# Performance work log

Measured on AMD Instinct MI355X. Metric: run time of the kernel, lower is better.

Reference implementation:

```python
import jax, jax.numpy as jnp
import numpy as np

N_NODES = 50000


def setup_inputs() -> dict:
    key = jax.random.key(0)
    k1, k2, k3, k4, k5 = jax.random.split(key, 5)
    x = jax.random.normal(k1, (N_NODES, 128), dtype=jnp.float32)
    edge_index = jax.random.randint(k2, (2, 800000), 0, N_NODES, dtype=jnp.int64)
    # Linear layers: torch Linear stores weight as [out, in]; init ~ U(-1/sqrt(in), 1/sqrt(in))
    s = 1.0 / np.sqrt(128.0)
    W_rel = jax.random.uniform(k3, (128, 128), dtype=jnp.float32, minval=-s, maxval=s)
    b_rel = jax.random.uniform(k4, (128,), dtype=jnp.float32, minval=-s, maxval=s)
    W_root = jax.random.uniform(k5, (128, 128), dtype=jnp.float32, minval=-s, maxval=s)
    return {"x": x, "edge_index": edge_index, "W_rel": W_rel, "b_rel": b_rel, "W_root": W_root}


def reference(x, edge_index, W_rel, b_rel, W_root):
    # GraphConv (PyG): out_i = W_rel @ (sum_{j -> i} x_j) + b_rel + W_root @ x_i
    src, dst = edge_index[0], edge_index[1]
    msgs = x[src]  # [E, in] gather
    agg = jax.ops.segment_sum(msgs, dst, num_segments=N_NODES)  # [N, in] scatter-add
    out = agg @ W_rel.T + b_rel + x @ W_root.T
    # ReLU; dropout_rate = DropoutRate.NONE -> p=0, identity
    return jax.nn.relu(out)
```

## Files before the change

### kernel.cpp

```cpp
#include <hip/hip_runtime.h>
#include <hip/hip_bf16.h>


#define F 128
#define NPB 32
#define NPARTS 8
#define CAP 128
#define CAPB 768
#define AST 68

typedef __bf16 bf16x8 __attribute__((ext_vector_type(8)));
typedef float f32x4 __attribute__((ext_vector_type(4)));

__device__ inline unsigned f32_to_bf16_rne(float f) {
  unsigned u = __float_as_uint(f);
  unsigned r = u + 0x7fffu + ((u >> 16) & 1u);
  return r >> 16;
}
__device__ inline unsigned pack2(float2 v) {
  return f32_to_bf16_rne(v.x) | (f32_to_bf16_rne(v.y) << 16);
}
__device__ inline unsigned pack2f(float a, float b) {
  return f32_to_bf16_rne(a) | (f32_to_bf16_rne(b) << 16);
}
__device__ inline void upk4(uint4 v, float* a) {
  a[0] += __uint_as_float(v.x << 16);
  a[1] += __uint_as_float(v.x & 0xffff0000u);
  a[2] += __uint_as_float(v.y << 16);
  a[3] += __uint_as_float(v.y & 0xffff0000u);
  a[4] += __uint_as_float(v.z << 16);
  a[5] += __uint_as_float(v.z & 0xffff0000u);
  a[6] += __uint_as_float(v.w << 16);
  a[7] += __uint_as_float(v.w & 0xffff0000u);
}

__global__ __launch_bounds__(256) void prep_bin2_kernel(
    const float4* __restrict__ x, const float2* __restrict__ w0,
    const float2* __restrict__ w1, const int* __restrict__ ei,
    uint2* __restrict__ xb2, unsigned* __restrict__ wb,
    int* __restrict__ binCursor, unsigned* __restrict__ bin,
    int E, int NB, int n4x, int n2w) {
  const int tid0 = blockIdx.x * 256 + threadIdx.x;
  const int stride = gridDim.x * 256;

  const int part = blockIdx.x & (NPARTS - 1);
  for (int e = tid0; e < E; e += stride) {
    unsigned src = (unsigned)ei[e];
    unsigned dst = (unsigned)ei[E + e];
    int cell = part * NB + (int)(dst >> 5);
    int slot = atomicAdd(&binCursor[cell], 1);
    if (slot < CAP) bin[(size_t)cell * CAP + slot] = (dst << 16) | src;
  }
  for (int i = tid0; i < n4x; i += stride) {
    float4 v = x[i];
    xb2[i] = make_uint2(pack2f(v.x, v.y), pack2f(v.z, v.w));
  }
  for (int i = tid0; i < 2 * n2w; i += stride)
    wb[i] = (i < n2w) ? pack2(w0[i]) : pack2(w1[i - n2w]);
}

__global__ __launch_bounds__(256) void agg_gemm2_kernel(
    const unsigned* __restrict__ xb, const unsigned* __restrict__ bin,
    const int* __restrict__ binCursor, const __bf16* __restrict__ wb,
    const float* __restrict__ brel, float* __restrict__ out, int N, int NB) {
  __shared__ int cntS[NPB];
  __shared__ int offS[NPB];
  __shared__ int curS[NPB];
  __shared__ unsigned short eLds[CAPB];
  __shared__ unsigned aLds[NPB * AST];

  const int b = blockIdx.x;
  const int t = threadIdx.x;
  if (t < NPB) cntS[t] = 0;
  __syncthreads();

  unsigned kreg[NPARTS];
  int cnt_p[NPARTS];
#pragma unroll
  for (int p = 0; p < NPARTS; ++p) {
    int cell = p * NB + b;
    int c = min(binCursor[cell], CAP);
    cnt_p[p] = c;
    kreg[p] = (t < c) ? bin[(size_t)cell * CAP + t] : 0u;
  }
#pragma unroll
  for (int p = 0; p < NPARTS; ++p) {
    if (t < cnt_p[p]) atomicAdd(&cntS[(kreg[p] >> 16) & (NPB - 1)], 1);
  }
  __syncthreads();

  if (t < 64) {
    int v = (t < NPB) ? cntS[t] : 0;
    int incl = v;
#pragma unroll
    for (int off = 1; off < NPB; off <<= 1) {
      int u = __shfl_up(incl, off);
      if (t >= off) incl += u;
    }
    if (t < NPB) {
      offS[t] = incl - v;
      curS[t] = incl - v;
    }
  }
  __syncthreads();

#pragma unroll
  for (int p = 0; p < NPARTS; ++p) {
    if (t < cnt_p[p]) {
      int d = (kreg[p] >> 16) & (NPB - 1);
      int pos = atomicAdd(&curS[d], 1);
      if (pos < CAPB) eLds[pos] = (unsigned short)(kreg[p] & 0xffffu);
    }
  }
  __syncthreads();

  const int wave = t >> 6;
  const int lane = t & 63;
  const int grp = lane >> 4;
  const int l16 = lane & 15;
  const uint4* __restrict__ xb4 = (const uint4*)xb;
  const int nodeBase = b * NPB;
  for (int di = wave; di < NPB; di += 4) {
    float a8[8] = {0.f, 0.f, 0.f, 0.f, 0.f, 0.f, 0.f, 0.f};
    int beg = min(offS[di], CAPB);
    int end = min(offS[di] + cntS[di], CAPB);
    int e = beg;
    for (; e + 16 <= end; e += 16) {
      int s0 = eLds[e + grp];
      int s1 = eLds[e + 4 + grp];
      int s2 = eLds[e + 8 + grp];
      int s3 = eLds[e + 12 + grp];
      uint4 v0 = xb4[(size_t)s0 * 16 + l16];
      uint4 v1 = xb4[(size_t)s1 * 16 + l16];
      uint4 v2 = xb4[(size_t)s2 * 16 + l16];
      uint4 v3 = xb4[(size_t)s3 * 16 + l16];
      upk4(v0, a8);
      upk4(v1, a8);
      upk4(v2, a8);
      upk4(v3, a8);
    }
    if (e + 8 <= end) {
      int s0 = eLds[e + grp];
      int s1 = eLds[e + 4 + grp];
      uint4 v0 = xb4[(size_t)s0 * 16 + l16];
      uint4 v1 = xb4[(size_t)s1 * 16 + l16];
      upk4(v0, a8);
      upk4(v1, a8);
      e += 8;
    }
    if (e < end) {
      int i0 = e + grp;
      int i1 = e + 4 + grp;
      if (i0 < end) {
        uint4 v0 = xb4[(size_t)eLds[i0] * 16 + l16];
        upk4(v0, a8);
      }
      if (i1 < end) {
        uint4 v1 = xb4[(size_t)eLds[i1] * 16 + l16];
        upk4(v1, a8);
      }
    }
#pragma unroll
    for (int j = 0; j < 8; ++j) {
      a8[j] += __shfl_xor(a8[j], 16);
      a8[j] += __shfl_xor(a8[j], 32);
    }
    if (grp == 0) {
      uint4 pk;
      pk.x = pack2f(a8[0], a8[1]);
      pk.y = pack2f(a8[2], a8[3]);
      pk.z = pack2f(a8[4], a8[5]);
      pk.w = pack2f(a8[6], a8[7]);
      *((uint4*)&aLds[di * AST + l16 * 4]) = pk;
    }
  }
  __syncthreads();

  const int m16 = lane & 15;
  const int quad = lane >> 4;
  const f32x4 zero4 = {0.f, 0.f, 0.f, 0.f};
  const bf16x8 zero8 = {};
  f32x4 acc[2][2];
#pragma unroll
  for (int mt = 0; mt < 2; ++mt)
#pragma unroll
    for (int s = 0; s < 2; ++s) acc[mt][s] = zero4;

#pragma unroll
  for (int ph = 0; ph < 2; ++ph) {
    const __bf16* __restrict__ W = wb + (size_t)ph * F * F;
#pragma unroll
    for (int k0 = 0; k0 < F; k0 += 32) {
      const int kcol = k0 + 8 * quad;
      bf16x8 a[2], bw[2];
#pragma unroll
      for (int mt = 0; mt < 2; ++mt) {
        if (ph == 0) {
          a[mt] = *(const bf16x8*)&aLds[(mt * 16 + m16) * AST + (kcol >> 1)];
        } else {
          int row = nodeBase + mt * 16 + m16;
          a[mt] = (row < N)
                      ? *(const bf16x8*)((const __bf16*)xb + (size_t)row * F + kcol)
                      : zero8;
        }
      }
#pragma unroll
      for (int s = 0; s < 2; ++s) {
        int nt = wave * 2 + s;
        bw[s] = *(const bf16x8*)(W + (size_t)(nt * 16 + m16) * F + kcol);
      }
#pragma unroll
      for (int mt = 0; mt < 2; ++mt)
#pragma unroll
        for (int s = 0; s < 2; ++s)
          acc[mt][s] = __builtin_amdgcn_mfma_f32_16x16x32_bf16(
              a[mt], bw[s], acc[mt][s], 0, 0, 0);
    }
  }

#pragma unroll
  for (int s = 0; s < 2; ++s) {
    int nt = wave * 2 + s;
    float bias = brel[nt * 16 + m16];
#pragma unroll
    for (int mt = 0; mt < 2; ++mt) {
      int row0 = nodeBase + mt * 16 + quad * 4;
#pragma unroll
      for (int r = 0; r < 4; ++r) {
        int row = row0 + r;
        if (row < N)
          out[(size_t)row * F + nt * 16 + m16] = fmaxf(acc[mt][s][r] + bias, 0.f);
      }
    }
  }
}

__global__ __launch_bounds__(256) void scatter_add_kernel(
    const float4* __restrict__ x4, const int* __restrict__ ei,
    float* __restrict__ agg, int E) {
  int gid = blockIdx.x * blockDim.x + threadIdx.x;
  if (gid >= E * 32) return;
  int e = gid >> 5, q = gid & 31;
  float4 v = x4[(size_t)ei[e] * 32 + q];
  float* a = agg + (size_t)ei[E + e] * F + q * 4;
  atomicAdd(a + 0, v.x);
  atomicAdd(a + 1, v.y);
  atomicAdd(a + 2, v.z);
  atomicAdd(a + 3, v.w);
}

#define ROWS_PER_BLOCK 64
#define SA_STRIDE 36
#define SW_STRIDE 132

__global__ __launch_bounds__(256) void gemm_fused_kernel(
    const float* __restrict__ agg, const float* __restrict__ x,
    const float* __restrict__ Wrel, const float* __restrict__ Wroot,
    const float* __restrict__ brel, float* __restrict__ out, int N) {
  __shared__ float sA[ROWS_PER_BLOCK * SA_STRIDE];
  __shared__ float sW[32 * SW_STRIDE];
  const int tid = threadIdx.x;
  const int j0 = (tid & 31) * 4;
  const int r0 = (tid >> 5) * 8;
  const int rowBase = blockIdx.x * ROWS_PER_BLOCK;
  float acc[8][4];
#pragma unroll
  for (int r = 0; r < 8; ++r)
#pragma unroll
    for (int c = 0; c < 4; ++c) acc[r][c] = 0.0f;
  for (int phase = 0; phase < 2; ++phase) {
    const float* __restrict__ A = phase ? x : agg;
    const float* __restrict__ W = phase ? Wroot : Wrel;
    for (int kc = 0; kc < F; kc += 32) {
#pragma unroll
      for (int idx = tid; idx < 512; idx += 256) {
        int row = idx >> 3, k4 = idx & 7;
        float4 v = make_float4(0.f, 0.f, 0.f, 0.f);
        int grow = rowBase + row;
        if (grow < N) v = *(const float4*)&A[(size_t)grow * F + kc + k4 * 4];
        *(float4*)&sA[row * SA_STRIDE + k4 * 4] = v;
      }
#pragma unroll
      for (int idx = tid; idx < 4096; idx += 256) {
        int j = idx >> 5, kk = idx & 31;
        sW[kk * SW_STRIDE + j] = W[j * F + kc + kk];
      }
      __syncthreads();
#pragma unroll
      for (int kk = 0; kk < 32; ++kk) {
        float4 w = *(const float4*)&sW[kk * SW_STRIDE + j0];
#pragma unroll
        for (int r = 0; r < 8; ++r) {
          float a = sA[(r0 + r) * SA_STRIDE + kk];
          acc[r][0] = fmaf(a, w.x, acc[r][0]);
          acc[r][1] = fmaf(a, w.y, acc[r][1]);
          acc[r][2] = fmaf(a, w.z, acc[r][2]);
          acc[r][3] = fmaf(a, w.w, acc[r][3]);
        }
      }
      __syncthreads();
    }
  }
  float b0 = brel[j0], b1 = brel[j0 + 1], b2 = brel[j0 + 2], b3 = brel[j0 + 3];
#pragma unroll
  for (int r = 0; r < 8; ++r) {
    int row = rowBase + r0 + r;
    if (row < N) {
      float4 v;
      v.x = fmaxf(acc[r][0] + b0, 0.0f);
      v.y = fmaxf(acc[r][1] + b1, 0.0f);
      v.z = fmaxf(acc[r][2] + b2, 0.0f);
      v.w = fmaxf(acc[r][3] + b3, 0.0f);
      *(float4*)&out[(size_t)row * F + j0] = v;
    }
  }
}

extern "C" void kernel_launch(void* const* d_in, const int* in_sizes, int n_in,
                              void* d_out, int out_size, void* d_ws, size_t ws_size,
                              hipStream_t stream) {
  const float* x     = (const float*)d_in[0];
  const int*   ei    = (const int*)d_in[1];
  const float* Wrel  = (const float*)d_in[2];
  const float* brel  = (const float*)d_in[3];
  const float* Wroot = (const float*)d_in[4];
  float* out = (float*)d_out;

  const int N = in_sizes[0] / F;
  const int E = in_sizes[1] / 2;
  const int NB = (N + NPB - 1) / NPB;

  size_t xbBytes  = ((size_t)N * F * 2 + 255) & ~(size_t)255;
  size_t wBytes   = ((size_t)2 * F * F * 2 + 255) & ~(size_t)255;
  size_t curBytes = ((size_t)NPARTS * NB * sizeof(int) + 255) & ~(size_t)255;
  size_t binBytes = ((size_t)NPARTS * NB * CAP * sizeof(unsigned) + 255) & ~(size_t)255;
  size_t needBin  = curBytes + binBytes + xbBytes + wBytes;

  if (ws_size >= needBin) {
    int*      binCursor = (int*)d_ws;
    unsigned* bin = (unsigned*)((char*)d_ws + curBytes);
    unsigned* xb  = (unsigned*)((char*)d_ws + curBytes + binBytes);
    unsigned* wb  = (unsigned*)((char*)d_ws + curBytes + binBytes + xbBytes);

    int n4x = N * (F / 4);
    int n2w = F * F / 2;

    hipMemsetAsync(binCursor, 0, (size_t)NPARTS * NB * sizeof(int), stream);
    prep_bin2_kernel<<<2048, 256, 0, stream>>>(
        (const float4*)x, (const float2*)Wrel, (const float2*)Wroot, ei,
        (uint2*)xb, wb, binCursor, bin, E, NB, n4x, n2w);
    agg_gemm2_kernel<<<NB, 256, 0, stream>>>(xb, bin, binCursor,
                                             (const __bf16*)wb, brel, out, N, NB);
  } else {
    hipMemsetAsync(out, 0, (size_t)N * F * sizeof(float), stream);
    long long total = (long long)E * 32;
    scatter_add_kernel<<<(int)((total + 255) / 256), 256, 0, stream>>>(
        (const float4*)x, ei, out, E);
    gemm_fused_kernel<<<(N + ROWS_PER_BLOCK - 1) / ROWS_PER_BLOCK, 256, 0,
                        stream>>>(out, x, Wrel, Wroot, brel, out, N);
  }
}
```

Baseline: 167.7 us.

## Compact bin loading across partitions and interleave two destination gathers per wave

Bin keys are now loaded as one compacted list spread over all 256 threads, up to four keys each, instead of each thread loading one slot per partition. This drops the requirement that partition counts stay within the thread count and keeps threads busy. The gather loop now handles two destination nodes per wave at once, issuing four independent row loads per iteration, to raise memory-level parallelism and hide latency. In exchange it uses more registers, and uneven degrees between the paired nodes fall back to serial drain loops.

```diff
diff --git a/kernel.cpp b/kernel.cpp
--- a/kernel.cpp
+++ b/kernel.cpp
@@ -34,6 +34,47 @@
   a[7] += __uint_as_float(v.w & 0xffff0000u);
 }
 
+__device__ inline void gather_drain(const uint4* __restrict__ xb4,
+                                    const unsigned short* __restrict__ eLds,
+                                    int e, int end, int grp, int l16,
+                                    float* a8) {
+  for (; e + 16 <= end; e += 16) {
+    int s0 = eLds[e + grp];
+    int s1 = eLds[e + 4 + grp];
+    int s2 = eLds[e + 8 + grp];
+    int s3 = eLds[e + 12 + grp];
+    uint4 v0 = xb4[(size_t)s0 * 16 + l16];
+    uint4 v1 = xb4[(size_t)s1 * 16 + l16];
+    uint4 v2 = xb4[(size_t)s2 * 16 + l16];
+    uint4 v3 = xb4[(size_t)s3 * 16 + l16];
+    upk4(v0, a8);
+    upk4(v1, a8);
+    upk4(v2, a8);
+    upk4(v3, a8);
+  }
+  if (e + 8 <= end) {
+    int s0 = eLds[e + grp];
+    int s1 = eLds[e + 4 + grp];
+    uint4 v0 = xb4[(size_t)s0 * 16 + l16];
+    uint4 v1 = xb4[(size_t)s1 * 16 + l16];
+    upk4(v0, a8);
+    upk4(v1, a8);
+    e += 8;
+  }
+  if (e < end) {
+    int i0 = e + grp;
+    int i1 = e + 4 + grp;
+    if (i0 < end) {
+      uint4 v0 = xb4[(size_t)eLds[i0] * 16 + l16];
+      upk4(v0, a8);
+    }
+    if (i1 < end) {
+      uint4 v1 = xb4[(size_t)eLds[i1] * 16 + l16];
+      upk4(v1, a8);
+    }
+  }
+}
+
 __global__ __launch_bounds__(256) void prep_bin2_kernel(
     const float4* __restrict__ x, const float2* __restrict__ w0,
     const float2* __restrict__ w1, const int* __restrict__ ei,
@@ -59,7 +100,7 @@
     wb[i] = (i < n2w) ? pack2(w0[i]) : pack2(w1[i - n2w]);
 }
 
-__global__ __launch_bounds__(256) void agg_gemm2_kernel(
+__global__ __launch_bounds__(256) void agg_gemm3_kernel(
     const unsigned* __restrict__ xb, const unsigned* __restrict__ bin,
     const int* __restrict__ binCursor, const __bf16* __restrict__ wb,
     const float* __restrict__ brel, float* __restrict__ out, int N, int NB) {
@@ -74,18 +115,32 @@
   if (t < NPB) cntS[t] = 0;
   __syncthreads();
 
-  unsigned kreg[NPARTS];
-  int cnt_p[NPARTS];
+  int partOff[NPARTS + 1];
+  partOff[0] = 0;
 #pragma unroll
   for (int p = 0; p < NPARTS; ++p) {
-    int cell = p * NB + b;
-    int c = min(binCursor[cell], CAP);
-    cnt_p[p] = c;
-    kreg[p] = (t < c) ? bin[(size_t)cell * CAP + t] : 0u;
-  }
-#pragma unroll
-  for (int p = 0; p < NPARTS; ++p) {
-    if (t < cnt_p[p]) atomicAdd(&cntS[(kreg[p] >> 16) & (NPB - 1)], 1);
+    int c = min(binCursor[p * NB + b], CAP);
+    partOff[p + 1] = partOff[p] + c;
+  }
+  const int total = partOff[NPARTS];
+
+  unsigned key[4];
+#pragma unroll
+  for (int r = 0; r < 4; ++r) {
+    int i = t + r * 256;
+    unsigned k = 0u;
+    if (i < total) {
+      int p = 0;
+#pragma unroll
+      for (int q = 1; q < NPARTS; ++q) p += (i >= partOff[q]);
+      int slot = i - partOff[p];
+      k = bin[(size_t)(p * NB + b) * CAP + slot];
+    }
+    key[r] = k;
+  }
+#pragma unroll
+  for (int r = 0; r < 4; ++r) {
+    if (t + r * 256 < total) atomicAdd(&cntS[(key[r] >> 16) & (NPB - 1)], 1);
   }
   __syncthreads();
 
@@ -105,11 +160,11 @@
   __syncthreads();
 
 #pragma unroll
-  for (int p = 0; p < NPARTS; ++p) {
-    if (t < cnt_p[p]) {
-      int d = (kreg[p] >> 16) & (NPB - 1);
+  for (int r = 0; r < 4; ++r) {
+    if (t + r * 256 < total) {
+      int d = (key[r] >> 16) & (NPB - 1);
       int pos = atomicAdd(&curS[d], 1);
-      if (pos < CAPB) eLds[pos] = (unsigned short)(kreg[p] & 0xffffu);
+      if (pos < CAPB) eLds[pos] = (unsigned short)(key[r] & 0xffffu);
     }
   }
   __syncthreads();
@@ -120,58 +175,54 @@
   const int l16 = lane & 15;
   const uint4* __restrict__ xb4 = (const uint4*)xb;
   const int nodeBase = b * NPB;
-  for (int di = wave; di < NPB; di += 4) {
+
+#pragma unroll
+  for (int j = 0; j < 4; ++j) {
+    const int dA = wave + 8 * j;
+    const int dB = dA + 4;
     float a8[8] = {0.f, 0.f, 0.f, 0.f, 0.f, 0.f, 0.f, 0.f};
-    int beg = min(offS[di], CAPB);
-    int end = min(offS[di] + cntS[di], CAPB);
-    int e = beg;
-    for (; e + 16 <= end; e += 16) {
-      int s0 = eLds[e + grp];
-      int s1 = eLds[e + 4 + grp];
-      int s2 = eLds[e + 8 + grp];
-      int s3 = eLds[e + 12 + grp];
-      uint4 v0 = xb4[(size_t)s0 * 16 + l16];
-      uint4 v1 = xb4[(size_t)s1 * 16 + l16];
-      uint4 v2 = xb4[(size_t)s2 * 16 + l16];
-      uint4 v3 = xb4[(size_t)s3 * 16 + l16];
-      upk4(v0, a8);
-      upk4(v1, a8);
-      upk4(v2, a8);
-      upk4(v3, a8);
-    }
-    if (e + 8 <= end) {
-      int s0 = eLds[e + grp];
-      int s1 = eLds[e + 4 + grp];
-      uint4 v0 = xb4[(size_t)s0 * 16 + l16];
-      uint4 v1 = xb4[(size_t)s1 * 16 + l16];
-      upk4(v0, a8);
-      upk4(v1, a8);
-      e += 8;
-    }
-    if (e < end) {
-      int i0 = e + grp;
-      int i1 = e + 4 + grp;
-      if (i0 < end) {
-        uint4 v0 = xb4[(size_t)eLds[i0] * 16 + l16];
-        upk4(v0, a8);
-      }
-      if (i1 < end) {
-        uint4 v1 = xb4[(size_t)eLds[i1] * 16 + l16];
-        upk4(v1, a8);
-      }
-    }
-#pragma unroll
-    for (int j = 0; j < 8; ++j) {
-      a8[j] += __shfl_xor(a8[j], 16);
-      a8[j] += __shfl_xor(a8[j], 32);
+    float b8[8] = {0.f, 0.f, 0.f, 0.f, 0.f, 0.f, 0.f, 0.f};
+    int eA = min(offS[dA], CAPB);
+    int endA = min(offS[dA] + cntS[dA], CAPB);
+    int eB = min(offS[dB], CAPB);
+    int endB = min(offS[dB] + cntS[dB], CAPB);
+    while (eA + 8 <= endA && eB + 8 <= endB) {
+      int sA0 = eLds[eA + grp];
+      int sA1 = eLds[eA + 4 + grp];
+      int sB0 = eLds[eB + grp];
+      int sB1 = eLds[eB + 4 + grp];
+      uint4 vA0 = xb4[(size_t)sA0 * 16 + l16];
+      uint4 vA1 = xb4[(size_t)sA1 * 16 + l16];
+      uint4 vB0 = xb4[(size_t)sB0 * 16 + l16];
+      uint4 vB1 = xb4[(size_t)sB1 * 16 + l16];
+      upk4(vA0, a8);
+      upk4(vA1, a8);
+      upk4(vB0, b8);
+      upk4(vB1, b8);
+      eA += 8;
+      eB += 8;
+    }
+    gather_drain(xb4, eLds, eA, endA, grp, l16, a8);
+    gather_drain(xb4, eLds, eB, endB, grp, l16, b8);
+#pragma unroll
+    for (int q = 0; q < 8; ++q) {
+      a8[q] += __shfl_xor(a8[q], 16);
+      b8[q] += __shfl_xor(b8[q], 16);
+      a8[q] += __shfl_xor(a8[q], 32);
+      b8[q] += __shfl_xor(b8[q], 32);
     }
     if (grp == 0) {
-      uint4 pk;
-      pk.x = pack2f(a8[0], a8[1]);
-      pk.y = pack2f(a8[2], a8[3]);
-      pk.z = pack2f(a8[4], a8[5]);
-      pk.w = pack2f(a8[6], a8[7]);
-      *((uint4*)&aLds[di * AST + l16 * 4]) = pk;
+      uint4 pkA, pkB;
+      pkA.x = pack2f(a8[0], a8[1]);
+      pkA.y = pack2f(a8[2], a8[3]);
+      pkA.z = pack2f(a8[4], a8[5]);
+      pkA.w = pack2f(a8[6], a8[7]);
+      pkB.x = pack2f(b8[0], b8[1]);
+      pkB.y = pack2f(b8[2], b8[3]);
+      pkB.z = pack2f(b8[4], b8[5]);
+      pkB.w = pack2f(b8[6], b8[7]);
+      *((uint4*)&aLds[dA * AST + l16 * 4]) = pkA;
+      *((uint4*)&aLds[dB * AST + l16 * 4]) = pkB;
     }
   }
   __syncthreads();
@@ -349,7 +400,7 @@
     prep_bin2_kernel<<<2048, 256, 0, stream>>>(
         (const float4*)x, (const float2*)Wrel, (const float2*)Wroot, ei,
         (uint2*)xb, wb, binCursor, bin, E, NB, n4x, n2w);
-    agg_gemm2_kernel<<<NB, 256, 0, stream>>>(xb, bin, binCursor,
+    agg_gemm3_kernel<<<NB, 256, 0, stream>>>(xb, bin, binCursor,
                                              (const __bf16*)wb, brel, out, N, NB);
   } else {
     hipMemsetAsync(out, 0, (size_t)N * F * sizeof(float), stream);
```

Measured after the change: 183.7 us. 9.6% more time.
